# Performance work log

Measured on AMD Instinct MI355X. Metric: run time of the kernel, lower is better.

The kernel has to match this reference:

```python
import jax, jax.numpy as jnp
import numpy as np

B = 32           # batch
LATENT = 512     # latent_dim
U = 256          # lstm_units
T = 2048


def setup_inputs() -> dict:
    key = jax.random.key(0)
    ks = jax.random.split(key, 8)
    s = lambda k, shape: jax.random.normal(k, shape, jnp.float32) * 0.05
    return {
        "context_vector": jax.random.normal(ks[0], (B, LATENT), jnp.float32),
        # context_dense: Dense(latent_dim -> lstm_units, relu)
        "Wc": s(ks[1], (LATENT, U)), "bc": jnp.zeros((U,), jnp.float32),
        # lstm1: input dim 2 (coords), keras gate order i,f,g,o in 4*U kernel
        "K1": s(ks[2], (2, 4 * U)), "R1": s(ks[3], (U, 4 * U)), "b1": jnp.zeros((4 * U,), jnp.float32),
        # lstm2: input dim U
        "K2": s(ks[4], (U, 4 * U)), "R2": s(ks[5], (U, 4 * U)), "b2": jnp.zeros((4 * U,), jnp.float32),
        # output_dense: Dense(lstm_units -> 2, sigmoid)
        "Wo": s(ks[6], (U, 2)), "bo": jnp.zeros((2,), jnp.float32),
    }


def _lstm_cell(x, h, c, K, R, b):
    # Keras LSTM cell: gates ordered [i, f, g, o]; sigmoid recurrent activation, tanh activation.
    z = x @ K + h @ R + b                      # [B, 4U]
    i, f, g, o = jnp.split(z, 4, axis=-1)
    c_new = jax.nn.sigmoid(f) * c + jax.nn.sigmoid(i) * jnp.tanh(g)
    h_new = jax.nn.sigmoid(o) * jnp.tanh(c_new)
    return h_new, c_new


def reference(context_vector, Wc, bc, K1, R1, b1, K2, R2, b2, Wo, bo):
    # initial states: h1 = relu(Dense(context)), c1 = h2 = c2 = 0
    h1 = jax.nn.relu(context_vector @ Wc + bc)           # [B, U]
    c1 = jnp.zeros_like(h1)
    h2 = jnp.zeros_like(h1)
    c2 = jnp.zeros_like(h1)
    start = jnp.full((context_vector.shape[0], 2), 0.5, context_vector.dtype)  # start token

    def step(carry, _):
        inp, h1, c1, h2, c2 = carry
        h1, c1 = _lstm_cell(inp, h1, c1, K1, R1, b1)
        h2, c2 = _lstm_cell(h1, h2, c2, K2, R2, b2)
        out = jax.nn.sigmoid(h2 @ Wo + bo)               # [B, 2]
        return (out, h1, c1, h2, c2), out

    _, ys = jax.lax.scan(step, (start, h1, c1, h2, c2), None, length=T)
    return jnp.transpose(ys, (1, 0, 2))                  # [B, T, 2]
```

## Files before the change

kernel.cpp:

```cpp
#include <hip/hip_runtime.h>


#define TSTEPS 2048
#define UNITS  256
#define NB     32
#define NSL    64
#define NTHR   512

constexpr int CH   = 72;
constexpr int VECF = 4 * CH;
constexpr int BUFW = 2 * 2 * VECF;
constexpr int SMEM_BYTES = 84 * 1024;

__device__ __forceinline__ float sigm(float x) { return 1.f / (1.f + expf(-x)); }

__device__ __forceinline__ float aload(const float* p) {
  return __hip_atomic_load(const_cast<float*>(p), __ATOMIC_RELAXED, __HIP_MEMORY_SCOPE_AGENT);
}
__device__ __forceinline__ int aloadi(const int* p) {
  return __hip_atomic_load(const_cast<int*>(p), __ATOMIC_RELAXED, __HIP_MEMORY_SCOPE_AGENT);
}
__device__ __forceinline__ void astore(float* p, float v) {
  __hip_atomic_store(p, v, __ATOMIC_RELAXED, __HIP_MEMORY_SCOPE_AGENT);
}
__device__ __forceinline__ void astorei(int* p, int v) {
  __hip_atomic_store(p, v, __ATOMIC_RELAXED, __HIP_MEMORY_SCOPE_AGENT);
}

__device__ __forceinline__ bool spin_ge(const int* flags, int lane, int target, bool prev_ok) {
  if (!prev_ok) return false;
  int guard = 0;
  while (true) {
    const int f = aloadi(flags + lane);
    if (__all(f >= target)) break;
    if (++guard > (1 << 20)) return false;
    __builtin_amdgcn_s_sleep(1);
  }
  asm volatile("" ::: "memory");
  return true;
}

__global__ __launch_bounds__(NTHR) void swd_kernel(
    const float* __restrict__ ctx, const float* __restrict__ Wc, const float* __restrict__ bc,
    const float* __restrict__ K1, const float* __restrict__ R1, const float* __restrict__ b1,
    const float* __restrict__ K2, const float* __restrict__ R2, const float* __restrict__ b2,
    const float* __restrict__ Wo, const float* __restrict__ bo,
    float* __restrict__ dout,
    int* __restrict__ flag1, int* __restrict__ flag2,
    float* __restrict__ ring1, float* __restrict__ ring2)
{
  extern __shared__ float sm[];
  const int wgid  = blockIdx.x;
  const int layer = wgid >> 7;
  const int half  = (wgid >> 6) & 1;
  const int slice = wgid & 63;
  const int tid  = threadIdx.x;
  const int lane = tid & 63;
  const int wid  = tid >> 6;
  const int c  = lane & 15;
  const int kk = lane >> 4;
  const int q  = c >> 2;
  const int u  = c & 3;
  const int gc = q * UNITS + slice * 4 + u;
  float* buf = sm + wid * BUFW;
  bool ok = true;

  if (layer == 0) {
    float w1[64];
    #pragma unroll
    for (int j = 0; j < 64; ++j) w1[j] = R1[(64 * kk + j) * 1024 + gc];
    const float k1a = K1[gc], k1b = K1[1024 + gc], bb1 = b1[gc];
    float wo[8];
    #pragma unroll
    for (int m = 0; m < 4; ++m) {
      wo[2 * m]     = Wo[(4 * lane + m) * 2];
      wo[2 * m + 1] = Wo[(4 * lane + m) * 2 + 1];
    }
    const float bo0 = bo[0], bo1 = bo[1];

    #pragma unroll
    for (int bi = 0; bi < 2; ++bi) {
      const int b = half * 16 + wid * 2 + bi;
      #pragma unroll
      for (int uu = 0; uu < 4; ++uu) {
        float p = 0.f;
        const float* cb = ctx + b * 512;
        const float* wc = Wc + slice * 4 + uu;
        #pragma unroll
        for (int m = 0; m < 8; ++m) {
          const int i = lane * 8 + m;
          p = fmaf(cb[i], wc[i * UNITS], p);
        }
        #pragma unroll
        for (int d = 32; d; d >>= 1) p += __shfl_down(p, d);
        if (lane == 0)
          astore(ring1 + b * UNITS + slice * 4 + uu, fmaxf(p + bc[slice * 4 + uu], 0.f));
      }
      asm volatile("s_waitcnt vmcnt(0)" ::: "memory");
      if (lane == 0) astorei(flag1 + b * NSL + slice, 1);
    }

    float c1a = 0.f, c1b = 0.f;
    for (int s = 0; s < TSTEPS; ++s) {
      #pragma unroll
      for (int bi = 0; bi < 2; ++bi) {
        const int b = half * 16 + wid * 2 + bi;
        float& c1 = bi ? c1b : c1a;
        float* bb = buf + bi * 2 * VECF;
        ok = spin_ge(flag1 + b * NSL, lane, s + 1, ok);
        const float* r1p = ring1 + ((s & 3) * NB + b) * UNITS + lane * 4;
        *(float4*)(bb + kk * CH + 4 * c) =
            make_float4(aload(r1p), aload(r1p + 1), aload(r1p + 2), aload(r1p + 3));
        float x0 = 0.5f, x1 = 0.5f;
        if (s > 0) {
          ok = spin_ge(flag2 + b * NSL, lane, s, ok);
          const float* r2p = ring2 + ((s & 3) * NB + b) * UNITS + lane * 4;
          const float g0 = aload(r2p), g1 = aload(r2p + 1), g2 = aload(r2p + 2), g3 = aload(r2p + 3);
          float po0 = g0 * wo[0] + g1 * wo[2] + g2 * wo[4] + g3 * wo[6];
          float po1 = g0 * wo[1] + g1 * wo[3] + g2 * wo[5] + g3 * wo[7];
          #pragma unroll
          for (int d = 1; d < 64; d <<= 1) { po0 += __shfl_xor(po0, d); po1 += __shfl_xor(po1, d); }
          x0 = sigm(po0 + bo0); x1 = sigm(po1 + bo1);
          if (slice == 0 && lane == 0)
            *(float2*)(dout + (b * TSTEPS + s - 1) * 2) = make_float2(x0, x1);
        }
        float ax = 0.f, ay = 0.f, az = 0.f, aw = 0.f;
        #pragma unroll
        for (int j = 0; j < 16; ++j) {
          const float4 hv = *(const float4*)(bb + kk * CH + 4 * j);
          ax = fmaf(w1[4 * j + 0], hv.x, ax);
          ay = fmaf(w1[4 * j + 1], hv.y, ay);
          az = fmaf(w1[4 * j + 2], hv.z, az);
          aw = fmaf(w1[4 * j + 3], hv.w, aw);
        }
        float part = (ax + ay) + (az + aw);
        part += __shfl_down(part, 16);
        part += __shfl_down(part, 32);
        const float z   = part + x0 * k1a + x1 * k1b + bb1;
        const float act = (q == 2) ? tanhf(z) : sigm(z);
        const float gi = __shfl(act, u),     gf = __shfl(act, 4 + u),
                    gg = __shfl(act, 8 + u), go = __shfl(act, 12 + u);
        if (lane < 4) {
          const float cn = gf * c1 + gi * gg;
          c1 = cn;
          astore(ring1 + (((s + 1) & 3) * NB + b) * UNITS + slice * 4 + lane, go * tanhf(cn));
        }
        asm volatile("s_waitcnt vmcnt(0)" ::: "memory");
        if (lane == 0) astorei(flag1 + b * NSL + slice, s + 2);
      }
    }
    if (slice == 0) {
      #pragma unroll
      for (int bi = 0; bi < 2; ++bi) {
        const int b = half * 16 + wid * 2 + bi;
        ok = spin_ge(flag2 + b * NSL, lane, TSTEPS, ok);
        const float* r2p = ring2 + ((TSTEPS & 3) * NB + b) * UNITS + lane * 4;
        const float g0 = aload(r2p), g1 = aload(r2p + 1), g2 = aload(r2p + 2), g3 = aload(r2p + 3);
        float po0 = g0 * wo[0] + g1 * wo[2] + g2 * wo[4] + g3 * wo[6];
        float po1 = g0 * wo[1] + g1 * wo[3] + g2 * wo[5] + g3 * wo[7];
        #pragma unroll
        for (int d = 1; d < 64; d <<= 1) { po0 += __shfl_xor(po0, d); po1 += __shfl_xor(po1, d); }
        if (lane == 0)
          *(float2*)(dout + (b * TSTEPS + TSTEPS - 1) * 2) =
              make_float2(sigm(po0 + bo0), sigm(po1 + bo1));
      }
    }
  } else {
    float wk[64], wr[64];
    #pragma unroll
    for (int j = 0; j < 64; ++j) {
      wk[j] = K2[(64 * kk + j) * 1024 + gc];
      wr[j] = R2[(64 * kk + j) * 1024 + gc];
    }
    const float bb2 = b2[gc];
    float c2a = 0.f, c2b = 0.f;
    for (int s = 0; s < TSTEPS; ++s) {
      #pragma unroll
      for (int bi = 0; bi < 2; ++bi) {
        const int b = half * 16 + wid * 2 + bi;
        float& c2 = bi ? c2b : c2a;
        float* bh1 = buf + bi * 2 * VECF;
        float* bh2 = bh1 + VECF;
        float g0 = 0.f, g1 = 0.f, g2 = 0.f, g3 = 0.f;
        if (s > 0) {
          ok = spin_ge(flag2 + b * NSL, lane, s, ok);
          const float* r2p = ring2 + ((s & 3) * NB + b) * UNITS + lane * 4;
          g0 = aload(r2p); g1 = aload(r2p + 1); g2 = aload(r2p + 2); g3 = aload(r2p + 3);
        }
        *(float4*)(bh2 + kk * CH + 4 * c) = make_float4(g0, g1, g2, g3);
        ok = spin_ge(flag1 + b * NSL, lane, s + 2, ok);
        const float* r1p = ring1 + (((s + 1) & 3) * NB + b) * UNITS + lane * 4;
        *(float4*)(bh1 + kk * CH + 4 * c) =
            make_float4(aload(r1p), aload(r1p + 1), aload(r1p + 2), aload(r1p + 3));
        float ax = 0.f, ay = 0.f, az = 0.f, aw = 0.f;
        #pragma unroll
        for (int j = 0; j < 16; ++j) {
          const float4 h1v = *(const float4*)(bh1 + kk * CH + 4 * j);
          const float4 h2v = *(const float4*)(bh2 + kk * CH + 4 * j);
          ax = fmaf(wk[4 * j + 0], h1v.x, ax);
          ay = fmaf(wk[4 * j + 1], h1v.y, ay);
          az = fmaf(wk[4 * j + 2], h1v.z, az);
          aw = fmaf(wk[4 * j + 3], h1v.w, aw);
          ax = fmaf(wr[4 * j + 0], h2v.x, ax);
          ay = fmaf(wr[4 * j + 1], h2v.y, ay);
          az = fmaf(wr[4 * j + 2], h2v.z, az);
          aw = fmaf(wr[4 * j + 3], h2v.w, aw);
        }
        float part = (ax + ay) + (az + aw);
        part += __shfl_down(part, 16);
        part += __shfl_down(part, 32);
        const float z   = part + bb2;
        const float act = (q == 2) ? tanhf(z) : sigm(z);
        const float gi = __shfl(act, u),     gf = __shfl(act, 4 + u),
                    gg = __shfl(act, 8 + u), go = __shfl(act, 12 + u);
        if (lane < 4) {
          const float cn = gf * c2 + gi * gg;
          c2 = cn;
          astore(ring2 + (((s + 1) & 3) * NB + b) * UNITS + slice * 4 + lane, go * tanhf(cn));
        }
        asm volatile("s_waitcnt vmcnt(0)" ::: "memory");
        if (lane == 0) astorei(flag2 + b * NSL + slice, s + 1);
      }
    }
  }
  (void)ok;
}

extern "C" void kernel_launch(void* const* d_in, const int* in_sizes, int n_in,
                              void* d_out, int out_size, void* d_ws, size_t ws_size,
                              hipStream_t stream) {
  (void)in_sizes; (void)n_in; (void)out_size; (void)ws_size;
  const float* ctx = (const float*)d_in[0];
  const float* Wc  = (const float*)d_in[1];
  const float* bc  = (const float*)d_in[2];
  const float* K1  = (const float*)d_in[3];
  const float* R1  = (const float*)d_in[4];
  const float* b1  = (const float*)d_in[5];
  const float* K2  = (const float*)d_in[6];
  const float* R2  = (const float*)d_in[7];
  const float* b2  = (const float*)d_in[8];
  const float* Wo  = (const float*)d_in[9];
  const float* bo  = (const float*)d_in[10];

  char* ws = (char*)d_ws;
  int*   flag1 = (int*)ws;
  int*   flag2 = flag1 + NB * NSL;
  float* ring1 = (float*)(ws + 2 * NB * NSL * sizeof(int));
  float* ring2 = ring1 + 4 * NB * UNITS;

  hipMemsetAsync(d_ws, 0, 2 * NB * NSL * sizeof(int), stream);
  hipFuncSetAttribute((const void*)swd_kernel,
                      hipFuncAttributeMaxDynamicSharedMemorySize, SMEM_BYTES);
  swd_kernel<<<dim3(256), dim3(NTHR), SMEM_BYTES, stream>>>(
      ctx, Wc, bc, K1, R1, b1, K2, R2, b2, Wo, bo,
      (float*)d_out, flag1, flag2, ring1, ring2);
}
```

Baseline: 28.18 ms.

## Replace flag-based handoff with checksum-tagged records and interleave batch pairs

Drops the separate per-slice flag arrays and the store-wait-flag sequence. Each slice now publishes a 4-float hidden record plus a checksum keyed to the step number in one write, and consumers poll the data itself until the checksum matches. Both batches of a wave are now polled and computed together, and layer 2 runs its recurrent matvec before waiting on layer 1. This is meant to cut synchronisation latency per step, but it depends on checksum collisions never occurring and on the two ring slots not being overwritten while still being read.

```diff
diff --git a/kernel.cpp b/kernel.cpp
--- a/kernel.cpp
+++ b/kernel.cpp
@@ -7,37 +7,65 @@
 #define NSL    64
 #define NTHR   512
 
+typedef float f4 __attribute__((ext_vector_type(4)));
+
 constexpr int CH   = 72;
 constexpr int VECF = 4 * CH;
-constexpr int BUFW = 2 * 2 * VECF;
+constexpr int BUFW = 4 * VECF;
 constexpr int SMEM_BYTES = 84 * 1024;
+constexpr int RECF = 8;
 
 __device__ __forceinline__ float sigm(float x) { return 1.f / (1.f + expf(-x)); }
 
-__device__ __forceinline__ float aload(const float* p) {
-  return __hip_atomic_load(const_cast<float*>(p), __ATOMIC_RELAXED, __HIP_MEMORY_SCOPE_AGENT);
-}
-__device__ __forceinline__ int aloadi(const int* p) {
-  return __hip_atomic_load(const_cast<int*>(p), __ATOMIC_RELAXED, __HIP_MEMORY_SCOPE_AGENT);
-}
-__device__ __forceinline__ void astore(float* p, float v) {
-  __hip_atomic_store(p, v, __ATOMIC_RELAXED, __HIP_MEMORY_SCOPE_AGENT);
-}
-__device__ __forceinline__ void astorei(int* p, int v) {
-  __hip_atomic_store(p, v, __ATOMIC_RELAXED, __HIP_MEMORY_SCOPE_AGENT);
-}
-
-__device__ __forceinline__ bool spin_ge(const int* flags, int lane, int target, bool prev_ok) {
-  if (!prev_ok) return false;
-  int guard = 0;
-  while (true) {
-    const int f = aloadi(flags + lane);
-    if (__all(f >= target)) break;
-    if (++guard > (1 << 20)) return false;
-    __builtin_amdgcn_s_sleep(1);
+__device__ __forceinline__ float mk_chk(float a, float b, float c, float d, float t) {
+  return __fadd_rn(__fadd_rn(__fadd_rn(__fadd_rn(a, b), c), d), t);
+}
+
+__device__ __forceinline__ void load_rec(const float* p, f4& a, float& chk) {
+  asm volatile("global_load_dwordx4 %0, %2, off sc0 sc1\n\t"
+               "global_load_dword %1, %2, off offset:16 sc0 sc1\n\t"
+               "s_waitcnt vmcnt(0)"
+               : "=&v"(a), "=&v"(chk) : "v"(p) : "memory");
+}
+__device__ __forceinline__ void store_rec(float* p, const f4& d, float chk) {
+  asm volatile("global_store_dwordx4 %0, %1, off sc0 sc1\n\t"
+               "global_store_dword %0, %2, off offset:16 sc0 sc1"
+               :: "v"(p), "v"(d), "v"(chk) : "memory");
+}
+
+__device__ __forceinline__ bool poll2(const float* p0, const float* p1, float tag,
+                                      f4& d0, f4& d1, bool ok) {
+  if (!ok) return false;
+  bool v0 = false, v1 = false;
+  int it = 0;
+  for (;;) {
+    if (!v0) {
+      f4 a; float cc; load_rec(p0, a, cc);
+      if (__float_as_uint(cc) == __float_as_uint(mk_chk(a.x, a.y, a.z, a.w, tag))) { d0 = a; v0 = true; }
+    }
+    if (!v1) {
+      f4 a; float cc; load_rec(p1, a, cc);
+      if (__float_as_uint(cc) == __float_as_uint(mk_chk(a.x, a.y, a.z, a.w, tag))) { d1 = a; v1 = true; }
+    }
+    if (__all(v0 && v1)) return true;
+    if (++it > (1 << 18)) return false;
+    if (it > 16) __builtin_amdgcn_s_sleep(1);
   }
-  asm volatile("" ::: "memory");
-  return true;
+}
+
+__device__ __forceinline__ void publish(float* ring, int k, int b, int slice,
+                                        int lane, float hn) {
+  const float h0 = __shfl(hn, 0), h1 = __shfl(hn, 1),
+              h2 = __shfl(hn, 2), h3 = __shfl(hn, 3);
+  const float chk = mk_chk(h0, h1, h2, h3, (float)k);
+  if (lane == 0) {
+    f4 d; d.x = h0; d.y = h1; d.z = h2; d.w = h3;
+    store_rec(ring + (((k & 1) * NB + b) * NSL + slice) * RECF, d, chk);
+  }
+}
+
+__device__ __forceinline__ const float* recp(const float* ring, int k, int b, int sl) {
+  return ring + (((k & 1) * NB + b) * NSL + sl) * RECF;
 }
 
 __global__ __launch_bounds__(NTHR) void swd_kernel(
@@ -45,23 +73,17 @@
     const float* __restrict__ K1, const float* __restrict__ R1, const float* __restrict__ b1,
     const float* __restrict__ K2, const float* __restrict__ R2, const float* __restrict__ b2,
     const float* __restrict__ Wo, const float* __restrict__ bo,
-    float* __restrict__ dout,
-    int* __restrict__ flag1, int* __restrict__ flag2,
-    float* __restrict__ ring1, float* __restrict__ ring2)
+    float* __restrict__ dout, float* __restrict__ ring1, float* __restrict__ ring2)
 {
   extern __shared__ float sm[];
   const int wgid  = blockIdx.x;
   const int layer = wgid >> 7;
   const int half  = (wgid >> 6) & 1;
   const int slice = wgid & 63;
-  const int tid  = threadIdx.x;
-  const int lane = tid & 63;
-  const int wid  = tid >> 6;
-  const int c  = lane & 15;
-  const int kk = lane >> 4;
-  const int q  = c >> 2;
-  const int u  = c & 3;
+  const int tid = threadIdx.x, lane = tid & 63, wid = tid >> 6;
+  const int c = lane & 15, kk = lane >> 4, q = c >> 2, u = c & 3;
   const int gc = q * UNITS + slice * 4 + u;
+  const int b0 = half * 16 + wid * 2, b1v = b0 + 1;
   float* buf = sm + wid * BUFW;
   bool ok = true;
 
@@ -70,99 +92,118 @@
     #pragma unroll
     for (int j = 0; j < 64; ++j) w1[j] = R1[(64 * kk + j) * 1024 + gc];
     const float k1a = K1[gc], k1b = K1[1024 + gc], bb1 = b1[gc];
-    float wo[8];
+    float wo0[4], wo1[4];
     #pragma unroll
     for (int m = 0; m < 4; ++m) {
-      wo[2 * m]     = Wo[(4 * lane + m) * 2];
-      wo[2 * m + 1] = Wo[(4 * lane + m) * 2 + 1];
+      wo0[m] = Wo[(4 * lane + m) * 2];
+      wo1[m] = Wo[(4 * lane + m) * 2 + 1];
     }
     const float bo0 = bo[0], bo1 = bo[1];
 
     #pragma unroll
     for (int bi = 0; bi < 2; ++bi) {
-      const int b = half * 16 + wid * 2 + bi;
+      const int b = b0 + bi;
+      float hv[4];
       #pragma unroll
       for (int uu = 0; uu < 4; ++uu) {
         float p = 0.f;
         const float* cb = ctx + b * 512;
         const float* wc = Wc + slice * 4 + uu;
         #pragma unroll
-        for (int m = 0; m < 8; ++m) {
-          const int i = lane * 8 + m;
-          p = fmaf(cb[i], wc[i * UNITS], p);
-        }
+        for (int m = 0; m < 8; ++m) p = fmaf(cb[lane * 8 + m], wc[(lane * 8 + m) * UNITS], p);
         #pragma unroll
         for (int d = 32; d; d >>= 1) p += __shfl_down(p, d);
-        if (lane == 0)
-          astore(ring1 + b * UNITS + slice * 4 + uu, fmaxf(p + bc[slice * 4 + uu], 0.f));
-      }
-      asm volatile("s_waitcnt vmcnt(0)" ::: "memory");
-      if (lane == 0) astorei(flag1 + b * NSL + slice, 1);
+        hv[uu] = fmaxf(p + bc[slice * 4 + uu], 0.f);
+      }
+      const float chk = mk_chk(hv[0], hv[1], hv[2], hv[3], 0.f);
+      if (lane == 0) {
+        f4 d; d.x = hv[0]; d.y = hv[1]; d.z = hv[2]; d.w = hv[3];
+        store_rec(ring1 + ((0 * NB + b) * NSL + slice) * RECF, d, chk);
+      }
     }
 
     float c1a = 0.f, c1b = 0.f;
+    float* bufA0 = buf;
+    float* bufA1 = buf + VECF;
     for (int s = 0; s < TSTEPS; ++s) {
-      #pragma unroll
-      for (int bi = 0; bi < 2; ++bi) {
-        const int b = half * 16 + wid * 2 + bi;
-        float& c1 = bi ? c1b : c1a;
-        float* bb = buf + bi * 2 * VECF;
-        ok = spin_ge(flag1 + b * NSL, lane, s + 1, ok);
-        const float* r1p = ring1 + ((s & 3) * NB + b) * UNITS + lane * 4;
-        *(float4*)(bb + kk * CH + 4 * c) =
-            make_float4(aload(r1p), aload(r1p + 1), aload(r1p + 2), aload(r1p + 3));
-        float x0 = 0.5f, x1 = 0.5f;
-        if (s > 0) {
-          ok = spin_ge(flag2 + b * NSL, lane, s, ok);
-          const float* r2p = ring2 + ((s & 3) * NB + b) * UNITS + lane * 4;
-          const float g0 = aload(r2p), g1 = aload(r2p + 1), g2 = aload(r2p + 2), g3 = aload(r2p + 3);
-          float po0 = g0 * wo[0] + g1 * wo[2] + g2 * wo[4] + g3 * wo[6];
-          float po1 = g0 * wo[1] + g1 * wo[3] + g2 * wo[5] + g3 * wo[7];
-          #pragma unroll
-          for (int d = 1; d < 64; d <<= 1) { po0 += __shfl_xor(po0, d); po1 += __shfl_xor(po1, d); }
-          x0 = sigm(po0 + bo0); x1 = sigm(po1 + bo1);
-          if (slice == 0 && lane == 0)
-            *(float2*)(dout + (b * TSTEPS + s - 1) * 2) = make_float2(x0, x1);
+      f4 d0, d1;
+      ok = poll2(recp(ring1, s, b0, lane), recp(ring1, s, b1v, lane), (float)s, d0, d1, ok);
+      *(f4*)(bufA0 + kk * CH + 4 * c) = d0;
+      *(f4*)(bufA1 + kk * CH + 4 * c) = d1;
+      float ax0 = 0.f, ay0 = 0.f, az0 = 0.f, aw0 = 0.f;
+      float ax1 = 0.f, ay1 = 0.f, az1 = 0.f, aw1 = 0.f;
+      #pragma unroll
+      for (int j = 0; j < 16; ++j) {
+        const f4 h0 = *(const f4*)(bufA0 + kk * CH + 4 * j);
+        const f4 h1 = *(const f4*)(bufA1 + kk * CH + 4 * j);
+        ax0 = fmaf(w1[4 * j + 0], h0.x, ax0); ay0 = fmaf(w1[4 * j + 1], h0.y, ay0);
+        az0 = fmaf(w1[4 * j + 2], h0.z, az0); aw0 = fmaf(w1[4 * j + 3], h0.w, aw0);
+        ax1 = fmaf(w1[4 * j + 0], h1.x, ax1); ay1 = fmaf(w1[4 * j + 1], h1.y, ay1);
+        az1 = fmaf(w1[4 * j + 2], h1.z, az1); aw1 = fmaf(w1[4 * j + 3], h1.w, aw1);
+      }
+      float part0 = (ax0 + ay0) + (az0 + aw0);
+      float part1 = (ax1 + ay1) + (az1 + aw1);
+      part0 += __shfl_down(part0, 16); part0 += __shfl_down(part0, 32);
+      part1 += __shfl_down(part1, 16); part1 += __shfl_down(part1, 32);
+      float x00 = 0.5f, x01 = 0.5f, x10 = 0.5f, x11 = 0.5f;
+      if (s > 0) {
+        f4 g0, g1;
+        ok = poll2(recp(ring2, s, b0, lane), recp(ring2, s, b1v, lane), (float)s, g0, g1, ok);
+        float po00 = g0.x * wo0[0] + g0.y * wo0[1] + g0.z * wo0[2] + g0.w * wo0[3];
+        float po01 = g0.x * wo1[0] + g0.y * wo1[1] + g0.z * wo1[2] + g0.w * wo1[3];
+        float po10 = g1.x * wo0[0] + g1.y * wo0[1] + g1.z * wo0[2] + g1.w * wo0[3];
+        float po11 = g1.x * wo1[0] + g1.y * wo1[1] + g1.z * wo1[2] + g1.w * wo1[3];
+        #pragma unroll
+        for (int d = 1; d < 64; d <<= 1) {
+          po00 += __shfl_xor(po00, d); po01 += __shfl_xor(po01, d);
+          po10 += __shfl_xor(po10, d); po11 += __shfl_xor(po11, d);
         }
-        float ax = 0.f, ay = 0.f, az = 0.f, aw = 0.f;
-        #pragma unroll
-        for (int j = 0; j < 16; ++j) {
-          const float4 hv = *(const float4*)(bb + kk * CH + 4 * j);
-          ax = fmaf(w1[4 * j + 0], hv.x, ax);
-          ay = fmaf(w1[4 * j + 1], hv.y, ay);
-          az = fmaf(w1[4 * j + 2], hv.z, az);
-          aw = fmaf(w1[4 * j + 3], hv.w, aw);
+        x00 = sigm(po00 + bo0); x01 = sigm(po01 + bo1);
+        x10 = sigm(po10 + bo0); x11 = sigm(po11 + bo1);
+        if (slice == 0 && lane == 0) {
+          *(float2*)(dout + (b0  * TSTEPS + s - 1) * 2) = make_float2(x00, x01);
+          *(float2*)(dout + (b1v * TSTEPS + s - 1) * 2) = make_float2(x10, x11);
         }
-        float part = (ax + ay) + (az + aw);
-        part += __shfl_down(part, 16);
-        part += __shfl_down(part, 32);
-        const float z   = part + x0 * k1a + x1 * k1b + bb1;
+      }
+      {
+        const float z = part0 + x00 * k1a + x01 * k1b + bb1;
         const float act = (q == 2) ? tanhf(z) : sigm(z);
         const float gi = __shfl(act, u),     gf = __shfl(act, 4 + u),
                     gg = __shfl(act, 8 + u), go = __shfl(act, 12 + u);
-        if (lane < 4) {
-          const float cn = gf * c1 + gi * gg;
-          c1 = cn;
-          astore(ring1 + (((s + 1) & 3) * NB + b) * UNITS + slice * 4 + lane, go * tanhf(cn));
-        }
-        asm volatile("s_waitcnt vmcnt(0)" ::: "memory");
-        if (lane == 0) astorei(flag1 + b * NSL + slice, s + 2);
+        const float cn = gf * c1a + gi * gg;
+        const float hn = go * tanhf(cn);
+        c1a = cn;
+        publish(ring1, s + 1, b0, slice, lane, hn);
+      }
+      {
+        const float z = part1 + x10 * k1a + x11 * k1b + bb1;
+        const float act = (q == 2) ? tanhf(z) : sigm(z);
+        const float gi = __shfl(act, u),     gf = __shfl(act, 4 + u),
+                    gg = __shfl(act, 8 + u), go = __shfl(act, 12 + u);
+        const float cn = gf * c1b + gi * gg;
+        const float hn = go * tanhf(cn);
+        c1b = cn;
+        publish(ring1, s + 1, b1v, slice, lane, hn);
       }
     }
     if (slice == 0) {
-      #pragma unroll
-      for (int bi = 0; bi < 2; ++bi) {
-        const int b = half * 16 + wid * 2 + bi;
-        ok = spin_ge(flag2 + b * NSL, lane, TSTEPS, ok);
-        const float* r2p = ring2 + ((TSTEPS & 3) * NB + b) * UNITS + lane * 4;
-        const float g0 = aload(r2p), g1 = aload(r2p + 1), g2 = aload(r2p + 2), g3 = aload(r2p + 3);
-        float po0 = g0 * wo[0] + g1 * wo[2] + g2 * wo[4] + g3 * wo[6];
-        float po1 = g0 * wo[1] + g1 * wo[3] + g2 * wo[5] + g3 * wo[7];
-        #pragma unroll
-        for (int d = 1; d < 64; d <<= 1) { po0 += __shfl_xor(po0, d); po1 += __shfl_xor(po1, d); }
-        if (lane == 0)
-          *(float2*)(dout + (b * TSTEPS + TSTEPS - 1) * 2) =
-              make_float2(sigm(po0 + bo0), sigm(po1 + bo1));
+      f4 g0, g1;
+      ok = poll2(recp(ring2, TSTEPS, b0, lane), recp(ring2, TSTEPS, b1v, lane),
+                 (float)TSTEPS, g0, g1, ok);
+      float po00 = g0.x * wo0[0] + g0.y * wo0[1] + g0.z * wo0[2] + g0.w * wo0[3];
+      float po01 = g0.x * wo1[0] + g0.y * wo1[1] + g0.z * wo1[2] + g0.w * wo1[3];
+      float po10 = g1.x * wo0[0] + g1.y * wo0[1] + g1.z * wo0[2] + g1.w * wo0[3];
+      float po11 = g1.x * wo1[0] + g1.y * wo1[1] + g1.z * wo1[2] + g1.w * wo1[3];
+      #pragma unroll
+      for (int d = 1; d < 64; d <<= 1) {
+        po00 += __shfl_xor(po00, d); po01 += __shfl_xor(po01, d);
+        po10 += __shfl_xor(po10, d); po11 += __shfl_xor(po11, d);
+      }
+      if (lane == 0) {
+        *(float2*)(dout + (b0  * TSTEPS + TSTEPS - 1) * 2) =
+            make_float2(sigm(po00 + bo0), sigm(po01 + bo1));
+        *(float2*)(dout + (b1v * TSTEPS + TSTEPS - 1) * 2) =
+            make_float2(sigm(po10 + bo0), sigm(po11 + bo1));
       }
     }
   } else {
@@ -174,52 +215,66 @@
     }
     const float bb2 = b2[gc];
     float c2a = 0.f, c2b = 0.f;
+    float* bh20 = buf;
+    float* bh21 = buf + VECF;
+    float* bh10 = buf + 2 * VECF;
+    float* bh11 = buf + 3 * VECF;
     for (int s = 0; s < TSTEPS; ++s) {
-      #pragma unroll
-      for (int bi = 0; bi < 2; ++bi) {
-        const int b = half * 16 + wid * 2 + bi;
-        float& c2 = bi ? c2b : c2a;
-        float* bh1 = buf + bi * 2 * VECF;
-        float* bh2 = bh1 + VECF;
-        float g0 = 0.f, g1 = 0.f, g2 = 0.f, g3 = 0.f;
-        if (s > 0) {
-          ok = spin_ge(flag2 + b * NSL, lane, s, ok);
-          const float* r2p = ring2 + ((s & 3) * NB + b) * UNITS + lane * 4;
-          g0 = aload(r2p); g1 = aload(r2p + 1); g2 = aload(r2p + 2); g3 = aload(r2p + 3);
-        }
-        *(float4*)(bh2 + kk * CH + 4 * c) = make_float4(g0, g1, g2, g3);
-        ok = spin_ge(flag1 + b * NSL, lane, s + 2, ok);
-        const float* r1p = ring1 + (((s + 1) & 3) * NB + b) * UNITS + lane * 4;
-        *(float4*)(bh1 + kk * CH + 4 * c) =
-            make_float4(aload(r1p), aload(r1p + 1), aload(r1p + 2), aload(r1p + 3));
-        float ax = 0.f, ay = 0.f, az = 0.f, aw = 0.f;
-        #pragma unroll
-        for (int j = 0; j < 16; ++j) {
-          const float4 h1v = *(const float4*)(bh1 + kk * CH + 4 * j);
-          const float4 h2v = *(const float4*)(bh2 + kk * CH + 4 * j);
-          ax = fmaf(wk[4 * j + 0], h1v.x, ax);
-          ay = fmaf(wk[4 * j + 1], h1v.y, ay);
-          az = fmaf(wk[4 * j + 2], h1v.z, az);
-          aw = fmaf(wk[4 * j + 3], h1v.w, aw);
-          ax = fmaf(wr[4 * j + 0], h2v.x, ax);
-          ay = fmaf(wr[4 * j + 1], h2v.y, ay);
-          az = fmaf(wr[4 * j + 2], h2v.z, az);
-          aw = fmaf(wr[4 * j + 3], h2v.w, aw);
-        }
-        float part = (ax + ay) + (az + aw);
-        part += __shfl_down(part, 16);
-        part += __shfl_down(part, 32);
-        const float z   = part + bb2;
+      f4 g0 = {0.f, 0.f, 0.f, 0.f}, g1 = {0.f, 0.f, 0.f, 0.f};
+      if (s > 0)
+        ok = poll2(recp(ring2, s, b0, lane), recp(ring2, s, b1v, lane), (float)s, g0, g1, ok);
+      *(f4*)(bh20 + kk * CH + 4 * c) = g0;
+      *(f4*)(bh21 + kk * CH + 4 * c) = g1;
+      float rx0 = 0.f, ry0 = 0.f, rz0 = 0.f, rw0 = 0.f;
+      float rx1 = 0.f, ry1 = 0.f, rz1 = 0.f, rw1 = 0.f;
+      #pragma unroll
+      for (int j = 0; j < 16; ++j) {
+        const f4 h0 = *(const f4*)(bh20 + kk * CH + 4 * j);
+        const f4 h1 = *(const f4*)(bh21 + kk * CH + 4 * j);
+        rx0 = fmaf(wr[4 * j + 0], h0.x, rx0); ry0 = fmaf(wr[4 * j + 1], h0.y, ry0);
+        rz0 = fmaf(wr[4 * j + 2], h0.z, rz0); rw0 = fmaf(wr[4 * j + 3], h0.w, rw0);
+        rx1 = fmaf(wr[4 * j + 0], h1.x, rx1); ry1 = fmaf(wr[4 * j + 1], h1.y, ry1);
+        rz1 = fmaf(wr[4 * j + 2], h1.z, rz1); rw1 = fmaf(wr[4 * j + 3], h1.w, rw1);
+      }
+      f4 d0, d1;
+      ok = poll2(recp(ring1, s + 1, b0, lane), recp(ring1, s + 1, b1v, lane),
+                 (float)(s + 1), d0, d1, ok);
+      *(f4*)(bh10 + kk * CH + 4 * c) = d0;
+      *(f4*)(bh11 + kk * CH + 4 * c) = d1;
+      float kx0 = 0.f, ky0 = 0.f, kz0 = 0.f, kw0 = 0.f;
+      float kx1 = 0.f, ky1 = 0.f, kz1 = 0.f, kw1 = 0.f;
+      #pragma unroll
+      for (int j = 0; j < 16; ++j) {
+        const f4 h0 = *(const f4*)(bh10 + kk * CH + 4 * j);
+        const f4 h1 = *(const f4*)(bh11 + kk * CH + 4 * j);
+        kx0 = fmaf(wk[4 * j + 0], h0.x, kx0); ky0 = fmaf(wk[4 * j + 1], h0.y, ky0);
+        kz0 = fmaf(wk[4 * j + 2], h0.z, kz0); kw0 = fmaf(wk[4 * j + 3], h0.w, kw0);
+        kx1 = fmaf(wk[4 * j + 0], h1.x, kx1); ky1 = fmaf(wk[4 * j + 1], h1.y, ky1);
+        kz1 = fmaf(wk[4 * j + 2], h1.z, kz1); kw1 = fmaf(wk[4 * j + 3], h1.w, kw1);
+      }
+      float part0 = ((rx0 + ry0) + (rz0 + rw0)) + ((kx0 + ky0) + (kz0 + kw0));
+      float part1 = ((rx1 + ry1) + (rz1 + rw1)) + ((kx1 + ky1) + (kz1 + kw1));
+      part0 += __shfl_down(part0, 16); part0 += __shfl_down(part0, 32);
+      part1 += __shfl_down(part1, 16); part1 += __shfl_down(part1, 32);
+      {
+        const float z = part0 + bb2;
         const float act = (q == 2) ? tanhf(z) : sigm(z);
         const float gi = __shfl(act, u),     gf = __shfl(act, 4 + u),
                     gg = __shfl(act, 8 + u), go = __shfl(act, 12 + u);
-        if (lane < 4) {
-          const float cn = gf * c2 + gi * gg;
-          c2 = cn;
-          astore(ring2 + (((s + 1) & 3) * NB + b) * UNITS + slice * 4 + lane, go * tanhf(cn));
-        }
-        asm volatile("s_waitcnt vmcnt(0)" ::: "memory");
-        if (lane == 0) astorei(flag2 + b * NSL + slice, s + 1);
+        const float cn = gf * c2a + gi * gg;
+        const float hn = go * tanhf(cn);
+        c2a = cn;
+        publish(ring2, s + 1, b0, slice, lane, hn);
+      }
+      {
+        const float z = part1 + bb2;
+        const float act = (q == 2) ? tanhf(z) : sigm(z);
+        const float gi = __shfl(act, u),     gf = __shfl(act, 4 + u),
+                    gg = __shfl(act, 8 + u), go = __shfl(act, 12 + u);
+        const float cn = gf * c2b + gi * gg;
+        const float hn = go * tanhf(cn);
+        c2b = cn;
+        publish(ring2, s + 1, b1v, slice, lane, hn);
       }
     }
   }
@@ -242,16 +297,12 @@
   const float* Wo  = (const float*)d_in[9];
   const float* bo  = (const float*)d_in[10];
 
-  char* ws = (char*)d_ws;
-  int*   flag1 = (int*)ws;
-  int*   flag2 = flag1 + NB * NSL;
-  float* ring1 = (float*)(ws + 2 * NB * NSL * sizeof(int));
-  float* ring2 = ring1 + 4 * NB * UNITS;
-
-  hipMemsetAsync(d_ws, 0, 2 * NB * NSL * sizeof(int), stream);
+  float* ring1 = (float*)d_ws;
+  float* ring2 = ring1 + 2 * NB * NSL * RECF;
+
   hipFuncSetAttribute((const void*)swd_kernel,
                       hipFuncAttributeMaxDynamicSharedMemorySize, SMEM_BYTES);
   swd_kernel<<<dim3(256), dim3(NTHR), SMEM_BYTES, stream>>>(
       ctx, Wc, bc, K1, R1, b1, K2, R2, b2, Wo, bo,
-      (float*)d_out, flag1, flag2, ring1, ring2);
-}
+      (float*)d_out, ring1, ring2);
+}
```

After: 30.75 ms. 1.09x slower.
